# Optimization experiments

Hardware: AMD Instinct MI355X
Metric: run time of the kernel (lower is better)

Reference implementation:

```python
import jax, jax.numpy as jnp
import numpy as np

NV, NE, NT = 20000, 40000, 30000
D, H, L = 512, 8, 2
HD = D // H
SCALE = float(np.sqrt(HD))
EV, EE, ET = 160000, 160000, 120000
LN_EPS = 1e-5


def _layer_norm(x, g, b):
    m = jnp.mean(x, axis=-1, keepdims=True)
    v = jnp.mean((x - m) ** 2, axis=-1, keepdims=True)
    return (x - m) * jax.lax.rsqrt(v + LN_EPS) * g + b


def _attn_layer(x, ei, W, b, g, bt):
    # x: [N, D]; ei: [2, E]; W: [4, D, D] (q,k,v,out); b: [4, D]
    n = x.shape[0]
    resid = x
    q = (x @ W[0] + b[0]).reshape(n, H, HD)
    k = (x @ W[1] + b[1]).reshape(n, H, HD)
    v = (x @ W[2] + b[2]).reshape(n, H, HD)
    src, dst = ei[0], ei[1]
    # per-edge scores: query at target, key at source (k[edge_index[1]] gather in original)
    scores = jnp.sum(q[dst] * k[src], axis=-1) / SCALE        # [E, H]
    # NOTE: original applies softmax over dim=0, i.e. globally over the edge axis
    w = jax.nn.softmax(scores, axis=0)                         # [E, H]
    msgs = w[:, :, None] * v[src]                              # [E, H, HD]
    out = jax.ops.segment_sum(msgs, dst, num_segments=n)      # [N, H, HD]
    out = out.reshape(n, D) @ W[3] + b[3]
    return _layer_norm(out + resid, g, bt)


def _attn_stack(x, ei, W, b, g, bt):
    for l in range(L):
        x = _attn_layer(x, ei, W[l], b[l], g[l], bt[l])
    return x


def setup_inputs() -> dict:
    key = jax.random.key(0)
    ks = jax.random.split(key, 16)
    inp = {}
    inp['vertices'] = jax.random.normal(ks[0], (NV, D), jnp.float32)
    inp['edge_features'] = jax.random.normal(ks[1], (NE, D), jnp.float32)
    inp['triangle_features'] = jax.random.normal(ks[2], (NT, D), jnp.float32)
    inp['v_embed'] = jax.random.normal(ks[3], (NV, D), jnp.float32)
    inp['e_embed'] = jax.random.normal(ks[4], (NE, D), jnp.float32)
    inp['t_embed'] = jax.random.normal(ks[5], (NT, D), jnp.float32)
    inp['v_pos'] = jax.random.normal(ks[6], (NV, D), jnp.float32) * 0.1
    inp['e_pos'] = jax.random.normal(ks[7], (NE, D), jnp.float32) * 0.1
    inp['t_pos'] = jax.random.normal(ks[8], (NT, D), jnp.float32) * 0.1
    for name, k2 in (('v', ks[9]), ('e', ks[10]), ('t', ks[11])):
        inp[name + 'W'] = jax.random.normal(k2, (L, 4, D, D), jnp.float32) * 0.02
        inp[name + 'B'] = jnp.zeros((L, 4, D), jnp.float32)
        inp[name + 'G'] = jnp.ones((L, D), jnp.float32)
        inp[name + 'Bt'] = jnp.zeros((L, D), jnp.float32)
    inp['head_W'] = jax.random.normal(ks[12], (3, D, D), jnp.float32) * 0.02
    inp['head_b'] = jnp.zeros((3, D), jnp.float32)
    inp['v_ei'] = jax.random.randint(ks[13], (2, EV), 0, NV, jnp.int32)
    inp['e_ei'] = jax.random.randint(ks[14], (2, EE), 0, NE, jnp.int32)
    inp['t_ei'] = jax.random.randint(ks[15], (2, ET), 0, NT, jnp.int32)
    return inp


def reference(vertices, edge_features, triangle_features, v_embed, e_embed, t_embed,
              v_pos, e_pos, t_pos, vW, vB, vG, vBt, eW, eB, eG, eBt,
              tW, tB, tG, tBt, head_W, head_b, v_ei, e_ei, t_ei):
    # embedding(arange(N)) == full table lookup; add positional params and input features
    v = v_embed + v_pos + vertices
    e = e_embed + e_pos + edge_features
    t = t_embed + t_pos + triangle_features
    v = _attn_stack(v, v_ei, vW, vB, vG, vBt)
    e = _attn_stack(e, e_ei, eW, eB, eG, eBt)
    t = _attn_stack(t, t_ei, tW, tB, tG, tBt)
    v_out = v @ head_W[0] + head_b[0]
    e_out = e @ head_W[1] + head_b[1]
    t_out = t @ head_W[2] + head_b[2]
    return (v_out, e_out, t_out)
```

## Files before the change

kernel.cpp:

```cpp
#include <hip/hip_runtime.h>


typedef __attribute__((ext_vector_type(8))) __bf16 bf16x8;
typedef __attribute__((ext_vector_type(4))) float f32x4;
typedef __attribute__((ext_vector_type(8))) unsigned short ushort8v;
typedef __attribute__((ext_vector_type(4))) unsigned short ushort4v;

__device__ __forceinline__ float b2f(unsigned short u) {
  union { unsigned u; float f; } x; x.u = (unsigned)u << 16; return x.f;
}
__device__ __forceinline__ unsigned short f2b(float f) {
  union { float f; unsigned u; } x; x.f = f;
  unsigned r = x.u + 0x7fffu + ((x.u >> 16) & 1u);
  return (unsigned short)(r >> 16);
}
__device__ __forceinline__ int xcd_swizzle(int orig, int nwg) {
  const int xcd = orig & 7, lin = orig >> 3;
  const int q = nwg >> 3, r8 = nwg & 7;
  return (xcd < r8 ? xcd * (q + 1) : r8 * (q + 1) + (xcd - r8) * q) + lin;
}
__device__ __forceinline__ void stage16(const void* g, void* lds_uniform) {
  __builtin_amdgcn_global_load_lds(
      (const __attribute__((address_space(1))) void*)g,
      (__attribute__((address_space(3))) void*)lds_uniform, 16, 0, 0);
}

struct IB {
  const float4* a[3]; const float4* b[3]; const float4* c[3];
  unsigned short* xb[3];
  long long cum[4];
};
struct HB {
  const int* ei[3]; int E[3]; int cum[4];
  int* deg[3]; const int* rowptr[3]; int* srcs[3];
};
struct PB {
  const int* deg[3]; int* rowptr[3]; int N[3]; int nbcum[4];
};
struct GB {
  const unsigned short* A[3]; const unsigned short* BT[3];
  const float* bias[3]; void* C[3];
  int M[3]; int cum[4];
};
struct SB {
  const unsigned short* qkv[3]; const int* srcs[3]; const int* rowptr[3];
  float* sc[3]; float* pm[3]; float* ps[3];
  int N[3]; int cum[4];
};
struct MB {
  const float* pm[3]; const float* ps[3]; int nslots[3];
};
struct AB {
  const unsigned short* qkv[3]; const float* sc[3]; const int* srcs[3];
  const int* rowptr[3]; unsigned short* agg[3];
  int N[3]; int cum[4];
};
struct LB {
  const unsigned short* proj[3]; const float* g[3]; const float* bt[3];
  unsigned short* xb[3]; int N[3]; int cum[4];
};
__device__ __forceinline__ int find3(int b, const int* cum) {
  return (b >= cum[1]) + (b >= cum[2]);
}

__global__ __launch_bounds__(256) void init_b_kernel(IB ib)
{
  long long total = ib.cum[3];
  long long stride = (long long)gridDim.x * 256;
  for (long long i = (long long)blockIdx.x * 256 + threadIdx.x; i < total; i += stride) {
    int s = (i >= ib.cum[1]) + (i >= ib.cum[2]);
    long long j = i - ib.cum[s];
    float4 av = ib.a[s][j], bv = ib.b[s][j], cv = ib.c[s][j];
    ushort4v o;
    o.x = f2b(av.x + bv.x + cv.x); o.y = f2b(av.y + bv.y + cv.y);
    o.z = f2b(av.z + bv.z + cv.z); o.w = f2b(av.w + bv.w + cv.w);
    *(ushort4v*)(ib.xb[s] + j * 4) = o;
  }
}

__global__ __launch_bounds__(256) void transpose_all_kernel(
    const float* W0, const float* W1, const float* W2, const float* Wh,
    unsigned short* WT)
{
  __shared__ float t[32][33];
  int z = blockIdx.z;
  const float* src = (z < 8)  ? W0 + (size_t)z * 262144
                   : (z < 16) ? W1 + (size_t)(z - 8) * 262144
                   : (z < 24) ? W2 + (size_t)(z - 16) * 262144
                              : Wh + (size_t)(z - 24) * 262144;
  unsigned short* dst = WT + (size_t)z * 262144;
  int bx = blockIdx.x * 32, by = blockIdx.y * 32;
  int tx = threadIdx.x, ty = threadIdx.y;
  #pragma unroll
  for (int i = 0; i < 32; i += 8)
    t[ty + i][tx] = src[(size_t)(by + ty + i) * 512 + bx + tx];
  __syncthreads();
  #pragma unroll
  for (int i = 0; i < 32; i += 8) {
    int c = bx + ty + i;
    int p = (c & ~0x3C) | ((c & 0x30) >> 2) | ((c & 0x0C) << 2);
    dst[(size_t)p * 512 + by + tx] = f2b(t[tx][ty + i]);
  }
}

template<int OUT_BF16>
__global__ __launch_bounds__(512, 2) void gemm_big_kernel(GB gb, int Ncols)
{
  constexpr int K = 512;
  __shared__ unsigned short smem[65536];

  const int b = blockIdx.x;
  const int s = find3(b, gb.cum);
  const int wgid = xcd_swizzle(b - gb.cum[s], gb.cum[s + 1] - gb.cum[s]);
  const unsigned short* A  = gb.A[s];
  const unsigned short* BT = gb.BT[s];
  const float* bias = gb.bias[s];
  const int M = gb.M[s];

  const int tiles_n = Ncols >> 8;
  const int tm = wgid / tiles_n;
  const int tn = wgid - tm * tiles_n;
  const int row0 = tm << 8, col0 = tn << 8;
  const int lane = threadIdx.x & 63, wid = threadIdx.x >> 6;
  const int wr = (wid >> 2) << 7;
  const int wc = (wid & 3) << 6;

  f32x4 acc[8][4];
  #pragma unroll
  for (int i = 0; i < 8; ++i)
    #pragma unroll
    for (int j = 0; j < 4; ++j) acc[i][j] = (f32x4)0.f;

  int srow[4], scsw[4], sseg[4];
  #pragma unroll
  for (int i = 0; i < 4; ++i) {
    int seg = (i << 3) | wid;
    int idx = (seg << 6) | lane;
    int row = idx >> 3, ch = idx & 7;
    sseg[i] = seg; srow[i] = row; scsw[i] = ch ^ (row & 7);
  }

  #define STG_PAIR(buf, kb_, i)                                               \
    { int ra = row0 + srow[i]; ra = (ra < M) ? ra : (M - 1);                  \
      stage16(A + (size_t)ra * K + (kb_) + (scsw[i] << 3),                    \
              smem + (buf) * 32768 + (sseg[i] << 9));                         \
      int rb = col0 + srow[i];                                                \
      stage16(BT + (size_t)rb * K + (kb_) + (scsw[i] << 3),                   \
              smem + (buf) * 32768 + 16384 + (sseg[i] << 9)); }

  STG_PAIR(0, 0, 0) STG_PAIR(0, 0, 1) STG_PAIR(0, 0, 2) STG_PAIR(0, 0, 3)
  __syncthreads();

  const int lm = lane & 15;
  const int kbl = (lane >> 4) << 4;

  #pragma unroll
  for (int kt = 0; kt < 8; ++kt) {
    const int cur = kt & 1, nxt = cur ^ 1, kb1 = (kt + 1) << 6;
    const char* Asb = (const char*)(smem + cur * 32768);
    const char* Bsb = Asb + 32768;

    auto rdA = [&](int mi, int kk) -> bf16x8 {
      int r = wr + (mi << 4) + lm;
      int kb = (kk << 6) + kbl;
      return *(const bf16x8*)(Asb + (r << 7) + (kb ^ ((r & 7) << 4)));
    };
    auto rdB = [&](int ni, int kk) -> bf16x8 {
      int r = wc + (ni << 4) + lm;
      int kb = (kk << 6) + kbl;
      return *(const bf16x8*)(Bsb + (r << 7) + (kb ^ ((r & 7) << 4)));
    };

    bf16x8 av[4], bv[4];

    #pragma unroll
    for (int i = 0; i < 4; ++i) { av[i] = rdA(i, 0); bv[i] = rdB(i, 0); }
    if (kt < 7) { STG_PAIR(nxt, kb1, 0) STG_PAIR(nxt, kb1, 1) }
    __builtin_amdgcn_s_barrier();
    __builtin_amdgcn_s_setprio(1);
    #pragma unroll
    for (int mi = 0; mi < 4; ++mi)
      #pragma unroll
      for (int ni = 0; ni < 4; ++ni)
        acc[mi][ni] = __builtin_amdgcn_mfma_f32_16x16x32_bf16(
            bv[ni], av[mi], acc[mi][ni], 0, 0, 0);
    __builtin_amdgcn_s_setprio(0);
    __builtin_amdgcn_s_barrier();

    #pragma unroll
    for (int i = 0; i < 4; ++i) av[i] = rdA(4 + i, 0);
    if (kt < 7) { STG_PAIR(nxt, kb1, 2) STG_PAIR(nxt, kb1, 3) }
    __builtin_amdgcn_s_barrier();
    __builtin_amdgcn_s_setprio(1);
    #pragma unroll
    for (int mi = 0; mi < 4; ++mi)
      #pragma unroll
      for (int ni = 0; ni < 4; ++ni)
        acc[4 + mi][ni] = __builtin_amdgcn_mfma_f32_16x16x32_bf16(
            bv[ni], av[mi], acc[4 + mi][ni], 0, 0, 0);
    __builtin_amdgcn_s_setprio(0);
    __builtin_amdgcn_s_barrier();

    #pragma unroll
    for (int i = 0; i < 4; ++i) { av[i] = rdA(i, 1); bv[i] = rdB(i, 1); }
    __builtin_amdgcn_s_barrier();
    __builtin_amdgcn_s_setprio(1);
    #pragma unroll
    for (int mi = 0; mi < 4; ++mi)
      #pragma unroll
      for (int ni = 0; ni < 4; ++ni)
        acc[mi][ni] = __builtin_amdgcn_mfma_f32_16x16x32_bf16(
            bv[ni], av[mi], acc[mi][ni], 0, 0, 0);
    __builtin_amdgcn_s_setprio(0);
    __builtin_amdgcn_s_barrier();

    #pragma unroll
    for (int i = 0; i < 4; ++i) av[i] = rdA(4 + i, 1);
    __builtin_amdgcn_s_barrier();
    __builtin_amdgcn_s_setprio(1);
    #pragma unroll
    for (int mi = 0; mi < 4; ++mi)
      #pragma unroll
      for (int ni = 0; ni < 4; ++ni)
        acc[4 + mi][ni] = __builtin_amdgcn_mfma_f32_16x16x32_bf16(
            bv[ni], av[mi], acc[4 + mi][ni], 0, 0, 0);
    __builtin_amdgcn_s_setprio(0);

    __syncthreads();
  }
  #undef STG_PAIR

  const int mrow = lane & 15;
  const int t4 = (lane >> 4) << 4;
  float bsv[16];
  #pragma unroll
  for (int ni = 0; ni < 4; ++ni) {
    float4 bvv = *(const float4*)(bias + col0 + wc + t4 + (ni << 2));
    bsv[4*ni+0] = bvv.x; bsv[4*ni+1] = bvv.y; bsv[4*ni+2] = bvv.z; bsv[4*ni+3] = bvv.w;
  }

  if (OUT_BF16) {
    unsigned short* C = (unsigned short*)gb.C[s];
    #pragma unroll
    for (int mi = 0; mi < 8; ++mi) {
      int rowg = row0 + wr + (mi << 4) + mrow;
      if (rowg < M) {
        ushort8v o0, o1;
        #pragma unroll
        for (int r = 0; r < 4; ++r) {
          o0[r]     = f2b(acc[mi][0][r] + bsv[r]);
          o0[4 + r] = f2b(acc[mi][1][r] + bsv[4 + r]);
          o1[r]     = f2b(acc[mi][2][r] + bsv[8 + r]);
          o1[4 + r] = f2b(acc[mi][3][r] + bsv[12 + r]);
        }
        unsigned short* cp = C + (size_t)rowg * Ncols + col0 + wc + t4;
        *(ushort8v*)cp = o0;
        *(ushort8v*)(cp + 8) = o1;
      }
    }
  } else {
    float* C = (float*)gb.C[s];
    #pragma unroll
    for (int mi = 0; mi < 8; ++mi) {
      int rowg = row0 + wr + (mi << 4) + mrow;
      if (rowg < M) {
        float* cp = C + (size_t)rowg * Ncols + col0 + wc + t4;
        #pragma unroll
        for (int ni = 0; ni < 4; ++ni) {
          float4 v;
          v.x = acc[mi][ni][0] + bsv[4*ni+0];
          v.y = acc[mi][ni][1] + bsv[4*ni+1];
          v.z = acc[mi][ni][2] + bsv[4*ni+2];
          v.w = acc[mi][ni][3] + bsv[4*ni+3];
          *(float4*)(cp + (ni << 2)) = v;
        }
      }
    }
  }
}

template<int OUT_BF16>
__global__ __launch_bounds__(256) void gemm_sm_kernel(GB gb, int Ncols)
{
  constexpr int K = 512;
  __shared__ unsigned short As[8192];
  __shared__ unsigned short Bs[8192];

  const int b = blockIdx.x;
  const int s = find3(b, gb.cum);
  const int wgid = xcd_swizzle(b - gb.cum[s], gb.cum[s + 1] - gb.cum[s]);
  const unsigned short* A  = gb.A[s];
  const unsigned short* BT = gb.BT[s];
  const float* bias = gb.bias[s];
  const int M = gb.M[s];

  const int tiles_n = Ncols >> 7;
  const int tm = wgid / tiles_n;
  const int tn = wgid - tm * tiles_n;
  const int row0 = tm << 7, col0 = tn << 7;
  const int lane = threadIdx.x & 63, wid = threadIdx.x >> 6;
  const int wm = (wid >> 1) << 6, wn = (wid & 1) << 6;

  f32x4 acc[4][4];
  #pragma unroll
  for (int i = 0; i < 4; ++i)
    #pragma unroll
    for (int j = 0; j < 4; ++j) acc[i][j] = (f32x4)0.f;

  int srow[4], scsw[4], sseg[4];
  #pragma unroll
  for (int i = 0; i < 4; ++i) {
    int seg = (i << 2) | wid;
    int idx = (seg << 6) | lane;
    int row = idx >> 3, ch = idx & 7;
    sseg[i] = seg; srow[i] = row; scsw[i] = ch ^ (row & 7);
  }

  #pragma unroll
  for (int kt = 0; kt < 8; ++kt) {
    const int kbase = kt << 6;
    #pragma unroll
    for (int i = 0; i < 4; ++i) {
      int ra = row0 + srow[i]; ra = (ra < M) ? ra : (M - 1);
      stage16(A + (size_t)ra * K + kbase + (scsw[i] << 3), As + (sseg[i] << 9));
      int rb = col0 + srow[i];
      stage16(BT + (size_t)rb * K + kbase + (scsw[i] << 3), Bs + (sseg[i] << 9));
    }
    asm volatile("s_waitcnt vmcnt(0)" ::: "memory");
    __syncthreads();

    #pragma unroll
    for (int kk = 0; kk < 2; ++kk) {
      const int kb = (kk << 6) + ((lane >> 4) << 4);
      bf16x8 af[4], bfr[4];
      #pragma unroll
      for (int mi = 0; mi < 4; ++mi) {
        int r = wm + (mi << 4) + (lane & 15);
        af[mi] = *(const bf16x8*)((const char*)As + (r << 7) + (kb ^ ((r & 7) << 4)));
      }
      #pragma unroll
      for (int ni = 0; ni < 4; ++ni) {
        int r = wn + (ni << 4) + (lane & 15);
        bfr[ni] = *(const bf16x8*)((const char*)Bs + (r << 7) + (kb ^ ((r & 7) << 4)));
      }
      #pragma unroll
      for (int mi = 0; mi < 4; ++mi)
        #pragma unroll
        for (int ni = 0; ni < 4; ++ni)
          acc[mi][ni] = __builtin_amdgcn_mfma_f32_16x16x32_bf16(
              bfr[ni], af[mi], acc[mi][ni], 0, 0, 0);
    }
    __syncthreads();
  }

  const int mrow = lane & 15;
  const int t4 = (lane >> 4) << 4;
  float bsv[16];
  #pragma unroll
  for (int ni = 0; ni < 4; ++ni) {
    float4 bvv = *(const float4*)(bias + col0 + wn + t4 + (ni << 2));
    bsv[4*ni+0] = bvv.x; bsv[4*ni+1] = bvv.y; bsv[4*ni+2] = bvv.z; bsv[4*ni+3] = bvv.w;
  }

  if (OUT_BF16) {
    unsigned short* C = (unsigned short*)gb.C[s];
    #pragma unroll
    for (int mi = 0; mi < 4; ++mi) {
      int rowg = row0 + wm + (mi << 4) + mrow;
      if (rowg < M) {
        ushort8v o0, o1;
        #pragma unroll
        for (int r = 0; r < 4; ++r) {
          o0[r]     = f2b(acc[mi][0][r] + bsv[r]);
          o0[4 + r] = f2b(acc[mi][1][r] + bsv[4 + r]);
          o1[r]     = f2b(acc[mi][2][r] + bsv[8 + r]);
          o1[4 + r] = f2b(acc[mi][3][r] + bsv[12 + r]);
        }
        unsigned short* cp = C + (size_t)rowg * Ncols + col0 + wn + t4;
        *(ushort8v*)cp = o0;
        *(ushort8v*)(cp + 8) = o1;
      }
    }
  } else {
    float* C = (float*)gb.C[s];
    #pragma unroll
    for (int mi = 0; mi < 4; ++mi) {
      int rowg = row0 + wm + (mi << 4) + mrow;
      if (rowg < M) {
        float* cp = C + (size_t)rowg * Ncols + col0 + wn + t4;
        #pragma unroll
        for (int ni = 0; ni < 4; ++ni) {
          float4 v;
          v.x = acc[mi][ni][0] + bsv[4*ni+0];
          v.y = acc[mi][ni][1] + bsv[4*ni+1];
          v.z = acc[mi][ni][2] + bsv[4*ni+2];
          v.w = acc[mi][ni][3] + bsv[4*ni+3];
          *(float4*)(cp + (ni << 2)) = v;
        }
      }
    }
  }
}

__global__ __launch_bounds__(256) void scores_b_kernel(SB sb)
{
  int b = blockIdx.x;
  int s = find3(b, sb.cum);
  int lb = b - sb.cum[s];
  const unsigned short* qkv = sb.qkv[s];
  const int* srcs = sb.srcs[s];
  float* sc = sb.sc[s];
  int wid = threadIdx.x >> 6, lane = threadIdx.x & 63;
  int n = (lb << 2) | wid;
  float mx = -1e30f, sm = 0.f;
  if (n < sb.N[s]) {
    int beg = sb.rowptr[s][n], end = sb.rowptr[s][n + 1];
    if (beg < end) {
      ushort8v qv = *(const ushort8v*)(qkv + (size_t)n * 1536 + (lane << 3));
      float qf[8];
      #pragma unroll
      for (int j = 0; j < 8; ++j) qf[j] = b2f(qv[j]);
      int i = beg;
      for (; i + 2 <= end; i += 2) {
        int s0 = srcs[i], s1 = srcs[i + 1];
        ushort8v k0 = *(const ushort8v*)(qkv + (size_t)s0 * 1536 + 512 + (lane << 3));
        ushort8v k1 = *(const ushort8v*)(qkv + (size_t)s1 * 1536 + 512 + (lane << 3));
        float p0 = 0.f, p1 = 0.f;
        #pragma unroll
        for (int j = 0; j < 8; ++j) { p0 += qf[j] * b2f(k0[j]); p1 += qf[j] * b2f(k1[j]); }
        p0 += __shfl_xor(p0, 1); p1 += __shfl_xor(p1, 1);
        p0 += __shfl_xor(p0, 2); p1 += __shfl_xor(p1, 2);
        p0 += __shfl_xor(p0, 4); p1 += __shfl_xor(p1, 4);
        p0 *= 0.125f; p1 *= 0.125f;
        float nm = fmaxf(mx, fmaxf(p0, p1));
        sm = sm * __expf(mx - nm) + __expf(p0 - nm) + __expf(p1 - nm);
        mx = nm;
        if (!(lane & 7)) {
          sc[(size_t)i * 8 + (lane >> 3)] = p0;
          sc[(size_t)(i + 1) * 8 + (lane >> 3)] = p1;
        }
      }
      if (i < end) {
        int s0 = srcs[i];
        ushort8v k0 = *(const ushort8v*)(qkv + (size_t)s0 * 1536 + 512 + (lane << 3));
        float p0 = 0.f;
        #pragma unroll
        for (int j = 0; j < 8; ++j) p0 += qf[j] * b2f(k0[j]);
        p0 += __shfl_xor(p0, 1);
        p0 += __shfl_xor(p0, 2);
        p0 += __shfl_xor(p0, 4);
        p0 *= 0.125f;
        float nm = fmaxf(mx, p0);
        sm = sm * __expf(mx - nm) + __expf(p0 - nm);
        mx = nm;
        if (!(lane & 7)) sc[(size_t)i * 8 + (lane >> 3)] = p0;
      }
    }
  }
  if (!(lane & 7)) {
    size_t slot = ((size_t)lb << 2) | wid;
    sb.pm[s][slot * 8 + (lane >> 3)] = mx;
    sb.ps[s][slot * 8 + (lane >> 3)] = sm;
  }
}

__device__ __forceinline__ void pair_reduce_block(
    float (&m)[8], float (&s)[8], float* redm, float* reds)
{
  int lane = threadIdx.x & 63, wid = threadIdx.x >> 6;
  #pragma unroll
  for (int h = 0; h < 8; ++h)
    #pragma unroll
    for (int off = 1; off < 64; off <<= 1) {
      float om = __shfl_xor(m[h], off);
      float os = __shfl_xor(s[h], off);
      float M = fmaxf(m[h], om);
      s[h] = s[h] * __expf(m[h] - M) + os * __expf(om - M);
      m[h] = M;
    }
  if (lane == 0) {
    #pragma unroll
    for (int h = 0; h < 8; ++h) { redm[h * 4 + wid] = m[h]; reds[h * 4 + wid] = s[h]; }
  }
  __syncthreads();
  if (threadIdx.x == 0) {
    #pragma unroll
    for (int h = 0; h < 8; ++h) {
      float M = redm[h * 4], S = reds[h * 4];
      #pragma unroll
      for (int w = 1; w < 4; ++w) {
        float om = redm[h * 4 + w], os = reds[h * 4 + w];
        float nM = fmaxf(M, om);
        S = S * __expf(M - nM) + os * __expf(om - nM);
        M = nM;
      }
      m[h] = M; s[h] = S;
    }
  }
}

__global__ __launch_bounds__(256) void gms_part_b_kernel(
    MB mb, float* pm2, float* ps2)
{
  __shared__ float redm[32], reds[32];
  int s = blockIdx.x >> 8, j = blockIdx.x & 255;
  const float* pm = mb.pm[s];
  const float* ps = mb.ps[s];
  float m[8], sv[8];
  #pragma unroll
  for (int h = 0; h < 8; ++h) { m[h] = -1e30f; sv[h] = 0.f; }
  for (int i = j * 256 + threadIdx.x; i < mb.nslots[s]; i += 65536) {
    #pragma unroll
    for (int h = 0; h < 8; ++h) {
      float mi = pm[(size_t)i * 8 + h], si = ps[(size_t)i * 8 + h];
      float M = fmaxf(m[h], mi);
      sv[h] = sv[h] * __expf(m[h] - M) + si * __expf(mi - M);
      m[h] = M;
    }
  }
  pair_reduce_block(m, sv, redm, reds);
  if (threadIdx.x == 0) {
    #pragma unroll
    for (int h = 0; h < 8; ++h) {
      pm2[(s * 256 + j) * 8 + h] = m[h];
      ps2[(s * 256 + j) * 8 + h] = sv[h];
    }
  }
}

__global__ __launch_bounds__(256) void gms_final_b_kernel(
    const float* pm2, const float* ps2, float* gmax, float* ginv)
{
  __shared__ float redm[32], reds[32];
  int s = blockIdx.x;
  float m[8], sv[8];
  #pragma unroll
  for (int h = 0; h < 8; ++h) {
    m[h]  = pm2[(s * 256 + threadIdx.x) * 8 + h];
    sv[h] = ps2[(s * 256 + threadIdx.x) * 8 + h];
  }
  pair_reduce_block(m, sv, redm, reds);
  if (threadIdx.x == 0) {
    #pragma unroll
    for (int h = 0; h < 8; ++h) { gmax[s * 8 + h] = m[h]; ginv[s * 8 + h] = 1.0f / sv[h]; }
  }
}

__global__ __launch_bounds__(256) void hist_b_kernel(HB hb)
{
  int b = blockIdx.x;
  int s = find3(b, hb.cum);
  int e = (b - hb.cum[s]) * 256 + threadIdx.x;
  if (e < hb.E[s]) atomicAdd(&hb.deg[s][hb.ei[s][hb.E[s] + e]], 1);
}

__global__ __launch_bounds__(1024) void scan_part_b_kernel(PB pb, int* bsums)
{
  __shared__ int wsum[16];
  int b = blockIdx.x;
  int s = (b >= pb.nbcum[1]) + (b >= pb.nbcum[2]);
  int lb = b - pb.nbcum[s];
  int i = lb * 1024 + threadIdx.x;
  int lane = threadIdx.x & 63, wid = threadIdx.x >> 6;
  int sv = (i < pb.N[s]) ? pb.deg[s][i] : 0;
  #pragma unroll
  for (int off = 1; off < 64; off <<= 1) {
    int t = __shfl_up(sv, off);
    if (lane >= off) sv += t;
  }
  if (lane == 63) wsum[wid] = sv;
  __syncthreads();
  if (threadIdx.x < 16) {
    int ws = wsum[threadIdx.x];
    #pragma unroll
    for (int off = 1; off < 16; off <<= 1) {
      int t = __shfl_up(ws, off);
      if (threadIdx.x >= off) ws += t;
    }
    wsum[threadIdx.x] = ws;
  }
  __syncthreads();
  if (wid > 0) sv += wsum[wid - 1];
  if (i < pb.N[s]) pb.rowptr[s][i + 1] = sv;
  if (threadIdx.x == 1023) bsums[s * 64 + lb] = sv;
}

__global__ __launch_bounds__(64) void scan_bsums_b_kernel(
    int* bsums, int nb0, int nb1, int nb2)
{
  int s = blockIdx.x;
  int nb = (s == 0) ? nb0 : (s == 1) ? nb1 : nb2;
  int* bs = bsums + s * 64;
  int lane = threadIdx.x;
  int v = (lane < nb) ? bs[lane] : 0;
  #pragma unroll
  for (int off = 1; off < 64; off <<= 1) {
    int t = __shfl_up(v, off);
    if (lane >= off) v += t;
  }
  int ex = __shfl_up(v, 1);
  if (lane == 0) ex = 0;
  if (lane < nb) bs[lane] = ex;
}

__global__ __launch_bounds__(1024) void scan_add_b_kernel(
    PB pb, const int* bsums)
{
  int b = blockIdx.x;
  int s = (b >= pb.nbcum[1]) + (b >= pb.nbcum[2]);
  int lb = b - pb.nbcum[s];
  int i = lb * 1024 + threadIdx.x;
  if (lb == 0 && threadIdx.x == 0) pb.rowptr[s][0] = 0;
  if (i < pb.N[s] && lb > 0) pb.rowptr[s][i + 1] += bsums[s * 64 + lb];
}

__global__ __launch_bounds__(256) void scatter_b_kernel(HB hb)
{
  int b = blockIdx.x;
  int s = find3(b, hb.cum);
  int e = (b - hb.cum[s]) * 256 + threadIdx.x;
  if (e < hb.E[s]) {
    const int* ei = hb.ei[s];
    int dst = ei[hb.E[s] + e];
    int pos = atomicAdd(&hb.deg[s][dst], 1);
    hb.srcs[s][hb.rowptr[s][dst] + pos] = ei[e];
  }
}

__global__ __launch_bounds__(256) void aggregate_b_kernel(
    AB ab, const float* gmaxg, const float* ginvg)
{
  int b = blockIdx.x;
  int s = find3(b, ab.cum);
  int lb = b - ab.cum[s];
  int wid = threadIdx.x >> 6, lane = threadIdx.x & 63;
  int n = (lb << 2) | wid;
  if (n >= ab.N[s]) return;
  const unsigned short* qkv = ab.qkv[s];
  const float* sc = ab.sc[s];
  const int* srcs = ab.srcs[s];
  int beg = ab.rowptr[s][n], end = ab.rowptr[s][n + 1];
  int h = lane >> 3;
  float gm  = gmaxg[s * 8 + h];
  float inv = ginvg[s * 8 + h];
  float acc[8] = {0.f,0.f,0.f,0.f,0.f,0.f,0.f,0.f};
  int i = beg;
  for (; i + 4 <= end; i += 4) {
    int s0 = srcs[i], s1 = srcs[i + 1], s2 = srcs[i + 2], s3 = srcs[i + 3];
    float w0 = __expf(sc[(size_t)i * 8 + h] - gm) * inv;
    float w1 = __expf(sc[(size_t)(i + 1) * 8 + h] - gm) * inv;
    float w2 = __expf(sc[(size_t)(i + 2) * 8 + h] - gm) * inv;
    float w3 = __expf(sc[(size_t)(i + 3) * 8 + h] - gm) * inv;
    ushort8v v0 = *(const ushort8v*)(qkv + (size_t)s0 * 1536 + 1024 + (lane << 3));
    ushort8v v1 = *(const ushort8v*)(qkv + (size_t)s1 * 1536 + 1024 + (lane << 3));
    ushort8v v2 = *(const ushort8v*)(qkv + (size_t)s2 * 1536 + 1024 + (lane << 3));
    ushort8v v3 = *(const ushort8v*)(qkv + (size_t)s3 * 1536 + 1024 + (lane << 3));
    #pragma unroll
    for (int j = 0; j < 8; ++j)
      acc[j] += (w0 * b2f(v0[j]) + w1 * b2f(v1[j]))
              + (w2 * b2f(v2[j]) + w3 * b2f(v3[j]));
  }
  for (; i < end; ++i) {
    int s0 = srcs[i];
    float w0 = __expf(sc[(size_t)i * 8 + h] - gm) * inv;
    ushort8v v0 = *(const ushort8v*)(qkv + (size_t)s0 * 1536 + 1024 + (lane << 3));
    #pragma unroll
    for (int j = 0; j < 8; ++j) acc[j] += w0 * b2f(v0[j]);
  }
  ushort8v o;
  #pragma unroll
  for (int j = 0; j < 8; ++j) o[j] = f2b(acc[j]);
  *(ushort8v*)(ab.agg[s] + (size_t)n * 512 + (lane << 3)) = o;
}

__global__ __launch_bounds__(256) void ln_b_kernel(LB lb_)
{
  int b = blockIdx.x;
  int s = find3(b, lb_.cum);
  int lb = b - lb_.cum[s];
  int wid = threadIdx.x >> 6, lane = threadIdx.x & 63;
  int n = (lb << 2) | wid;
  if (n >= lb_.N[s]) return;
  size_t base = (size_t)n * 512 + (lane << 3);
  ushort8v pv = *(const ushort8v*)(lb_.proj[s] + base);
  ushort8v xv = *(const ushort8v*)(lb_.xb[s] + base);
  float y[8];
  #pragma unroll
  for (int j = 0; j < 8; ++j) y[j] = b2f(pv[j]) + b2f(xv[j]);
  float sum = 0.f;
  #pragma unroll
  for (int j = 0; j < 8; ++j) sum += y[j];
  #pragma unroll
  for (int off = 1; off < 64; off <<= 1) sum += __shfl_xor(sum, off);
  float mean = sum * (1.f / 512.f);
  float vs = 0.f;
  #pragma unroll
  for (int j = 0; j < 8; ++j) { float d = y[j] - mean; vs += d * d; }
  #pragma unroll
  for (int off = 1; off < 64; off <<= 1) vs += __shfl_xor(vs, off);
  float rstd = rsqrtf(vs * (1.f / 512.f) + 1e-5f);
  int gi = lane << 3;
  ushort8v ob;
  #pragma unroll
  for (int j = 0; j < 8; ++j)
    ob[j] = f2b((y[j] - mean) * rstd * lb_.g[s][gi + j] + lb_.bt[s][gi + j]);
  *(ushort8v*)(lb_.xb[s] + base) = ob;
}

extern "C" void kernel_launch(void* const* d_in, const int* in_sizes, int n_in,
                              void* d_out, int out_size, void* d_ws, size_t ws_size,
                              hipStream_t stream)
{
  (void)n_in; (void)out_size;
  const float* feat[3] = {(const float*)d_in[0], (const float*)d_in[1], (const float*)d_in[2]};
  const float* emb[3]  = {(const float*)d_in[3], (const float*)d_in[4], (const float*)d_in[5]};
  const float* pos[3]  = {(const float*)d_in[6], (const float*)d_in[7], (const float*)d_in[8]};
  const float* W[3]  = {(const float*)d_in[9],  (const float*)d_in[13], (const float*)d_in[17]};
  const float* Bb[3] = {(const float*)d_in[10], (const float*)d_in[14], (const float*)d_in[18]};
  const float* G[3]  = {(const float*)d_in[11], (const float*)d_in[15], (const float*)d_in[19]};
  const float* Bt[3] = {(const float*)d_in[12], (const float*)d_in[16], (const float*)d_in[20]};
  const float* headW = (const float*)d_in[21];
  const float* headB = (const float*)d_in[22];
  const int* ei[3] = {(const int*)d_in[23], (const int*)d_in[24], (const int*)d_in[25]};

  int Ns[3], Es[3];
  for (int s = 0; s < 3; ++s) { Ns[s] = in_sizes[s] / 512; Es[s] = in_sizes[23 + s] / 2; }

  long long Noff[4] = {0}, Eoff[4] = {0}, Roff[4] = {0}, Poff[4] = {0};
  for (int s = 0; s < 3; ++s) {
    Noff[s + 1] = Noff[s] + Ns[s];
    Eoff[s + 1] = Eoff[s] + Es[s];
    Roff[s + 1] = Roff[s] + Ns[s] + 1;
    Poff[s + 1] = Poff[s] + ((Ns[s] + 3) / 4) * 4;
  }

  char* base = (char*)d_ws;
  size_t off = 0;
  auto carve = [&](size_t bytes) -> char* {
    char* r = base + off;
    off += (bytes + 255) & ~(size_t)255;
    return r;
  };
  unsigned short* WT   = (unsigned short*)carve((size_t)27 * 262144 * 2);
  unsigned short* XB   = (unsigned short*)carve((size_t)Noff[3] * 512 * 2);
  unsigned short* QKV  = (unsigned short*)carve((size_t)Noff[3] * 1536 * 2);
  float*          SC   = (float*)carve((size_t)Eoff[3] * 8 * 4);
  unsigned short* AGG  = (unsigned short*)carve((size_t)Noff[3] * 512 * 2);
  int*   ROWPTR = (int*)carve((size_t)Roff[3] * 4);
  int*   DEG    = (int*)carve((size_t)Noff[3] * 4);
  int*   SRCS   = (int*)carve((size_t)Eoff[3] * 4);
  int*   BSUMS  = (int*)carve(3 * 64 * 4);
  float* PARTM  = (float*)carve((size_t)Poff[3] * 8 * 4);
  float* PARTS1 = (float*)carve((size_t)Poff[3] * 8 * 4);
  float* PARTM2 = (float*)carve(3 * 256 * 8 * 4);
  float* PARTS2 = (float*)carve(3 * 256 * 8 * 4);
  float* GMAX   = (float*)carve(256);
  float* GINV   = (float*)carve(256);
  if (off > ws_size) return;

  unsigned short* XBs[3];  unsigned short* QKVs[3]; float* SCs[3];
  unsigned short* AGGs[3]; int* ROWPTRs[3]; int* DEGs[3]; int* SRCSs[3];
  float* PMs[3]; float* PSs[3];
  for (int s = 0; s < 3; ++s) {
    XBs[s]  = XB  + Noff[s] * 512;
    QKVs[s] = QKV + Noff[s] * 1536;
    SCs[s]  = SC  + Eoff[s] * 8;
    AGGs[s] = AGG + Noff[s] * 512;
    ROWPTRs[s] = ROWPTR + Roff[s];
    DEGs[s] = DEG + Noff[s];
    SRCSs[s] = SRCS + Eoff[s];
    PMs[s] = PARTM + Poff[s] * 8;
    PSs[s] = PARTS1 + Poff[s] * 8;
  }

  transpose_all_kernel<<<dim3(16, 16, 27), dim3(32, 8), 0, stream>>>(
      W[0], W[1], W[2], headW, WT);

  IB ib;
  for (int s = 0; s < 3; ++s) {
    ib.a[s] = (const float4*)feat[s]; ib.b[s] = (const float4*)emb[s];
    ib.c[s] = (const float4*)pos[s];  ib.xb[s] = XBs[s];
  }
  ib.cum[0] = 0;
  for (int s = 0; s < 3; ++s) ib.cum[s + 1] = ib.cum[s] + (long long)Ns[s] * 128;
  init_b_kernel<<<2048, 256, 0, stream>>>(ib);

  HB hb;
  hb.cum[0] = 0;
  for (int s = 0; s < 3; ++s) {
    hb.ei[s] = ei[s]; hb.E[s] = Es[s];
    hb.cum[s + 1] = hb.cum[s] + (Es[s] + 255) / 256;
    hb.deg[s] = DEGs[s]; hb.rowptr[s] = ROWPTRs[s]; hb.srcs[s] = SRCSs[s];
  }
  PB pb;
  pb.nbcum[0] = 0;
  for (int s = 0; s < 3; ++s) {
    pb.deg[s] = DEGs[s]; pb.rowptr[s] = ROWPTRs[s]; pb.N[s] = Ns[s];
    pb.nbcum[s + 1] = pb.nbcum[s] + (Ns[s] + 1023) / 1024;
  }
  hipMemsetAsync(DEG, 0, (size_t)Noff[3] * 4, stream);
  hist_b_kernel<<<hb.cum[3], 256, 0, stream>>>(hb);
  scan_part_b_kernel<<<pb.nbcum[3], 1024, 0, stream>>>(pb, BSUMS);
  scan_bsums_b_kernel<<<3, 64, 0, stream>>>(
      BSUMS, (Ns[0] + 1023) / 1024, (Ns[1] + 1023) / 1024, (Ns[2] + 1023) / 1024);
  scan_add_b_kernel<<<pb.nbcum[3], 1024, 0, stream>>>(pb, BSUMS);
  hipMemsetAsync(DEG, 0, (size_t)Noff[3] * 4, stream);
  scatter_b_kernel<<<hb.cum[3], 256, 0, stream>>>(hb);

  int nsbcum[4] = {0}, mtcum[4] = {0}, mtscum[4] = {0};
  for (int s = 0; s < 3; ++s) {
    nsbcum[s + 1] = nsbcum[s] + (Ns[s] + 3) / 4;
    mtcum[s + 1]  = mtcum[s]  + ((Ns[s] + 255) >> 8) * 6;
    mtscum[s + 1] = mtscum[s] + ((Ns[s] + 127) >> 7) * 4;
  }

  MB mb;
  for (int s = 0; s < 3; ++s) {
    mb.pm[s] = PMs[s]; mb.ps[s] = PSs[s];
    mb.nslots[s] = ((Ns[s] + 3) / 4) * 4;
  }

  for (int l = 0; l < 2; ++l) {
    GB qg;
    for (int s = 0; s < 3; ++s) {
      qg.A[s] = XBs[s];
      qg.BT[s] = WT + (size_t)(s * 8 + l * 4) * 262144;
      qg.bias[s] = Bb[s] + (size_t)l * 2048;
      qg.C[s] = QKVs[s];
      qg.M[s] = Ns[s];
      qg.cum[s] = mtcum[s];
    }
    qg.cum[3] = mtcum[3];
    gemm_big_kernel<1><<<mtcum[3], 512, 0, stream>>>(qg, 1536);

    SB sb;
    for (int s = 0; s < 3; ++s) {
      sb.qkv[s] = QKVs[s]; sb.srcs[s] = SRCSs[s]; sb.rowptr[s] = ROWPTRs[s];
      sb.sc[s] = SCs[s]; sb.pm[s] = PMs[s]; sb.ps[s] = PSs[s];
      sb.N[s] = Ns[s]; sb.cum[s] = nsbcum[s];
    }
    sb.cum[3] = nsbcum[3];
    scores_b_kernel<<<nsbcum[3], 256, 0, stream>>>(sb);

    gms_part_b_kernel<<<768, 256, 0, stream>>>(mb, PARTM2, PARTS2);
    gms_final_b_kernel<<<3, 256, 0, stream>>>(PARTM2, PARTS2, GMAX, GINV);

    AB ab;
    for (int s = 0; s < 3; ++s) {
      ab.qkv[s] = QKVs[s]; ab.sc[s] = SCs[s]; ab.srcs[s] = SRCSs[s];
      ab.rowptr[s] = ROWPTRs[s]; ab.agg[s] = AGGs[s];
      ab.N[s] = Ns[s]; ab.cum[s] = nsbcum[s];
    }
    ab.cum[3] = nsbcum[3];
    aggregate_b_kernel<<<nsbcum[3], 256, 0, stream>>>(ab, GMAX, GINV);

    GB pg;
    for (int s = 0; s < 3; ++s) {
      pg.A[s] = AGGs[s];
      pg.BT[s] = WT + (size_t)(s * 8 + l * 4 + 3) * 262144;
      pg.bias[s] = Bb[s] + (size_t)(l * 2048 + 1536);
      pg.C[s] = QKVs[s];
      pg.M[s] = Ns[s];
      pg.cum[s] = mtscum[s];
    }
    pg.cum[3] = mtscum[3];
    gemm_sm_kernel<1><<<mtscum[3], 256, 0, stream>>>(pg, 512);

    LB lb;
    for (int s = 0; s < 3; ++s) {
      lb.proj[s] = QKVs[s]; lb.g[s] = G[s] + (size_t)l * 512;
      lb.bt[s] = Bt[s] + (size_t)l * 512; lb.xb[s] = XBs[s];
      lb.N[s] = Ns[s]; lb.cum[s] = nsbcum[s];
    }
    lb.cum[3] = nsbcum[3];
    ln_b_kernel<<<nsbcum[3], 256, 0, stream>>>(lb);
  }

  GB hg;
  size_t out_off = 0;
  for (int s = 0; s < 3; ++s) {
    hg.A[s] = XBs[s];
    hg.BT[s] = WT + (size_t)(24 + s) * 262144;
    hg.bias[s] = headB + (size_t)s * 512;
    hg.C[s] = (float*)d_out + out_off;
    hg.M[s] = Ns[s];
    hg.cum[s] = mtscum[s];
    out_off += (size_t)Ns[s] * 512;
  }
  hg.cum[3] = mtscum[3];
  gemm_sm_kernel<0><<<mtscum[3], 256, 0, stream>>>(hg, 512);
}
```

Measured before the change: 1.220 ms.

## Triple-buffer A tiles in big GEMM with partial vmcnt waits

The big GEMM kernel's shared-memory staging becomes 3 buffers for A and 2 for B. A tiles are prefetched two k-steps ahead. The end-of-iteration __syncthreads is replaced by s_waitcnt vmcnt(4) plus a barrier, so one stage of loads stays in flight across iterations. This raises LDS use from 128KB to 160KB per workgroup, which with launch_bounds(512,2) may cut occupancy to one workgroup per CU and relies on hand-counted outstanding loads.

```diff
diff --git a/kernel.cpp b/kernel.cpp
--- a/kernel.cpp
+++ b/kernel.cpp
@@ -107,7 +107,7 @@
 __global__ __launch_bounds__(512, 2) void gemm_big_kernel(GB gb, int Ncols)
 {
   constexpr int K = 512;
-  __shared__ unsigned short smem[65536];
+  __shared__ unsigned short smem[81920];
 
   const int b = blockIdx.x;
   const int s = find3(b, gb.cum);
@@ -140,25 +140,29 @@
     sseg[i] = seg; srow[i] = row; scsw[i] = ch ^ (row & 7);
   }
 
-  #define STG_PAIR(buf, kb_, i)                                               \
+  #define STG_A(buf3, kb_, i)                                                 \
     { int ra = row0 + srow[i]; ra = (ra < M) ? ra : (M - 1);                  \
       stage16(A + (size_t)ra * K + (kb_) + (scsw[i] << 3),                    \
-              smem + (buf) * 32768 + (sseg[i] << 9));                         \
-      int rb = col0 + srow[i];                                                \
+              smem + (buf3) * 16384 + (sseg[i] << 9)); }
+  #define STG_B(buf2, kb_, i)                                                 \
+    { int rb = col0 + srow[i];                                                \
       stage16(BT + (size_t)rb * K + (kb_) + (scsw[i] << 3),                   \
-              smem + (buf) * 32768 + 16384 + (sseg[i] << 9)); }
-
-  STG_PAIR(0, 0, 0) STG_PAIR(0, 0, 1) STG_PAIR(0, 0, 2) STG_PAIR(0, 0, 3)
-  __syncthreads();
+              smem + 49152 + (buf2) * 16384 + (sseg[i] << 9)); }
+
+  STG_B(0, 0, 0) STG_B(0, 0, 1) STG_B(0, 0, 2) STG_B(0, 0, 3)
+  STG_A(0, 0, 0) STG_A(0, 0, 1) STG_A(0, 0, 2) STG_A(0, 0, 3)
+  STG_A(1, 64, 0) STG_A(1, 64, 1) STG_A(1, 64, 2) STG_A(1, 64, 3)
+  asm volatile("s_waitcnt vmcnt(4)" ::: "memory");
+  __builtin_amdgcn_s_barrier();
 
   const int lm = lane & 15;
   const int kbl = (lane >> 4) << 4;
 
   #pragma unroll
   for (int kt = 0; kt < 8; ++kt) {
-    const int cur = kt & 1, nxt = cur ^ 1, kb1 = (kt + 1) << 6;
-    const char* Asb = (const char*)(smem + cur * 32768);
-    const char* Bsb = Asb + 32768;
+    const char* Asb = (const char*)(smem + (kt % 3) * 16384);
+    const char* Bsb = (const char*)(smem + 49152 + (kt & 1) * 16384);
+    const int kb1 = (kt + 1) << 6, kb2 = (kt + 2) << 6;
 
     auto rdA = [&](int mi, int kk) -> bf16x8 {
       int r = wr + (mi << 4) + lm;
@@ -175,7 +179,10 @@
 
     #pragma unroll
     for (int i = 0; i < 4; ++i) { av[i] = rdA(i, 0); bv[i] = rdB(i, 0); }
-    if (kt < 7) { STG_PAIR(nxt, kb1, 0) STG_PAIR(nxt, kb1, 1) }
+    if (kt < 7) {
+      STG_B((kt + 1) & 1, kb1, 0) STG_B((kt + 1) & 1, kb1, 1)
+      STG_B((kt + 1) & 1, kb1, 2) STG_B((kt + 1) & 1, kb1, 3)
+    }
     __builtin_amdgcn_s_barrier();
     __builtin_amdgcn_s_setprio(1);
     #pragma unroll
@@ -189,7 +196,10 @@
 
     #pragma unroll
     for (int i = 0; i < 4; ++i) av[i] = rdA(4 + i, 0);
-    if (kt < 7) { STG_PAIR(nxt, kb1, 2) STG_PAIR(nxt, kb1, 3) }
+    if (kt < 6) {
+      STG_A((kt + 2) % 3, kb2, 0) STG_A((kt + 2) % 3, kb2, 1)
+      STG_A((kt + 2) % 3, kb2, 2) STG_A((kt + 2) % 3, kb2, 3)
+    }
     __builtin_amdgcn_s_barrier();
     __builtin_amdgcn_s_setprio(1);
     #pragma unroll
@@ -226,9 +236,16 @@
             bv[ni], av[mi], acc[4 + mi][ni], 0, 0, 0);
     __builtin_amdgcn_s_setprio(0);
 
-    __syncthreads();
-  }
-  #undef STG_PAIR
+    if (kt < 6) {
+      asm volatile("s_waitcnt vmcnt(4) lgkmcnt(0)" ::: "memory");
+      __builtin_amdgcn_s_barrier();
+    } else if (kt == 6) {
+      asm volatile("s_waitcnt vmcnt(0) lgkmcnt(0)" ::: "memory");
+      __builtin_amdgcn_s_barrier();
+    }
+  }
+  #undef STG_A
+  #undef STG_B
 
   const int mrow = lane & 15;
   const int t4 = (lane >> 4) << 4;
```

Result: no change. 1.206 ms (-1.1%).
